# Kernel optimization log

Hardware: AMD Instinct MI355X
Metric: run time of the kernel (lower is better)

The kernel has to match this reference:

```python
import jax, jax.numpy as jnp
import numpy as np

SCALE = 768.0  # scale = output_features


def setup_inputs() -> dict:
    key = jax.random.key(0)
    k1, k2, k3, k4 = jax.random.split(key, 4)
    B, S, D, F = 8, 2048, 768, 768
    x = jax.random.normal(k1, (B, S, D), dtype=jnp.float32)
    # torch nn.Linear weights: shape (out_features, in_features), y = x @ W.T
    Wq = jax.random.normal(k2, (F, D), dtype=jnp.float32) * (1.0 / np.sqrt(D))
    Wk = jax.random.normal(k3, (F, D), dtype=jnp.float32) * (1.0 / np.sqrt(D))
    Wv = jax.random.normal(k4, (F, D), dtype=jnp.float32) * (1.0 / np.sqrt(D))
    return {"x": x, "Wq": Wq, "Wk": Wk, "Wv": Wv}


def _cdist_l2(q, k):
    # pairwise Euclidean distances, [B, S, S]; matches torch.cdist(q, k, p=2)
    q2 = jnp.sum(q * q, axis=-1)  # [B, S]
    k2 = jnp.sum(k * k, axis=-1)  # [B, S]
    qk = jnp.einsum('bid,bjd->bij', q, k)  # [B, S, S]
    d2 = q2[:, :, None] + k2[:, None, :] - 2.0 * qk
    return jnp.sqrt(jnp.maximum(d2, 0.0))


def reference(x, Wq, Wk, Wv):
    q = jnp.einsum('bsd,fd->bsf', x, Wq)
    k = jnp.einsum('bsd,fd->bsf', x, Wk)
    v = jnp.einsum('bsd,fd->bsf', x, Wv)
    scores = _cdist_l2(q, k) / jnp.sqrt(jnp.asarray(SCALE, dtype=x.dtype))
    attn = jax.nn.softmax(scores, axis=-1)  # NOTE: source softmaxes raw distances (no negation)
    return jnp.einsum('bij,bjf->bif', attn, v)
```

## Files before the change

kernel.cpp:

```cpp
#include <hip/hip_runtime.h>
#include <hip/hip_fp8.h>
#include <stdint.h>
#include <math.h>


typedef __attribute__((ext_vector_type(8))) __bf16 bf16x8;
typedef __attribute__((ext_vector_type(4))) float f32x4;
typedef __attribute__((ext_vector_type(4))) unsigned int u32x4;

__device__ __forceinline__ unsigned short f2b(float f) {
    unsigned u = __float_as_uint(f);
    unsigned r = 0x7fffu + ((u >> 16) & 1u);
    return (unsigned short)((u + r) >> 16);
}
__device__ __forceinline__ float b2f(unsigned short h) {
    return __uint_as_float(((unsigned)h) << 16);
}
__device__ __forceinline__ unsigned char f2f8(float f) {
    __hip_fp8_e4m3 t(f);
    return t.__x;
}
__device__ __forceinline__ float f8tof(unsigned char b) {
    int e = (b >> 3) & 15, m = b & 7;
    float v = e ? ldexpf(8.0f + m, e - 10) : ldexpf((float)m, -9);
    return (b & 0x80) ? -v : v;
}

__device__ __forceinline__ void wg_barrier() {
    asm volatile("" ::: "memory");
    __builtin_amdgcn_s_barrier();
    asm volatile("" ::: "memory");
}

__device__ __forceinline__ unsigned lds_off(const void* p) {
    return (unsigned)(uintptr_t)(const __attribute__((address_space(3))) char*)p;
}

__global__ __launch_bounds__(256) void castk(const float* __restrict__ src,
                                             unsigned short* __restrict__ dst, int n4) {
    int i = blockIdx.x * 256 + threadIdx.x;
    if (i >= n4) return;
    float4 v = ((const float4*)src)[i];
    ushort4 o;
    o.x = f2b(v.x); o.y = f2b(v.y); o.z = f2b(v.z); o.w = f2b(v.w);
    ((ushort4*)dst)[i] = o;
}

template <int MODE>
__global__ __launch_bounds__(256) void rowreduce(const unsigned short* __restrict__ X,
                                                 int L, int rows, float* __restrict__ out) {
    int w = threadIdx.x >> 6, lane = threadIdx.x & 63;
    int row = blockIdx.x * 4 + w;
    if (row >= rows) return;
    const unsigned short* xr = X + (size_t)row * L;
    float s = 0.f;
    int passes = L >> 8;
    for (int p = 0; p < passes; ++p) {
        ushort4 u = *(const ushort4*)(xr + (p << 8) + lane * 4);
        float a = b2f(u.x), b = b2f(u.y), c = b2f(u.z), d = b2f(u.w);
        s += MODE ? (a * a + b * b + c * c + d * d) : (a + b + c + d);
    }
#pragma unroll
    for (int o = 32; o > 0; o >>= 1) s += __shfl_down(s, o);
    if (lane == 0) out[row] = s;
}

__global__ __launch_bounds__(256) void rowreduce8(const unsigned char* __restrict__ X,
                                                  int L, int rows, float* __restrict__ out) {
    int w = threadIdx.x >> 6, lane = threadIdx.x & 63;
    int row = blockIdx.x * 4 + w;
    if (row >= rows) return;
    const unsigned char* xr = X + (size_t)row * L;
    float s = 0.f;
    int passes = L >> 8;
    for (int p = 0; p < passes; ++p) {
        uchar4 u = *(const uchar4*)(xr + (p << 8) + lane * 4);
        float a = f8tof(u.x), b = f8tof(u.y), c = f8tof(u.z), d = f8tof(u.w);
        s += a * a + b * b + c * c + d * d;
    }
#pragma unroll
    for (int o = 32; o > 0; o >>= 1) s += __shfl_down(s, o);
    if (lane == 0) out[row] = s;
}

#define MF(A_, B_, C_) (C_) = __builtin_amdgcn_mfma_f32_16x16x32_bf16((A_), (B_), (C_), 0, 0, 0)
#define MF8(A_, B_, C_) (C_) = __builtin_amdgcn_mfma_f32_16x16x32_fp8_fp8((A_), (B_), (C_), 0, 0, 0)
#define DSR(dst_, a_, imm_) \
    asm volatile("ds_read_b128 %0, %1 offset:" #imm_ : "=v"(dst_) : "v"(a_))
#define DSR64(dst_, a_, imm_) \
    asm volatile("ds_read_b64 %0, %1 offset:" #imm_ : "=v"(dst_) : "v"(a_))
#define GL4(d_, p_) asm volatile("global_load_dwordx4 %0, %1, off" : "=v"(d_) : "v"(p_))
#define DSW(a_, imm_, d_) \
    asm volatile("ds_write_b128 %0, %1 offset:" #imm_ :: "v"(a_), "v"(d_) : "memory")
#define LGKM(n_) asm volatile("s_waitcnt lgkmcnt(" #n_ ")" ::: "memory")
#define VMC0 asm volatile("s_waitcnt vmcnt(0)" ::: "memory")
#define SB0 __builtin_amdgcn_sched_barrier(0)

#define LOADT(T_) do {                                                     \
    const size_t ko_ = (size_t)(T_) * 64;                                  \
    GL4(ra0, pa + ko_);             GL4(ra1, pa + lda64 + ko_);            \
    GL4(ra2, pa + 2 * lda64 + ko_); GL4(ra3, pa + 3 * lda64 + ko_);        \
    GL4(rb0, pb + ko_);             GL4(rb1, pb + ldb64 + ko_);            \
    GL4(rb2, pb + 2 * ldb64 + ko_); GL4(rb3, pb + 3 * ldb64 + ko_);        \
} while (0)
#define WRITET(WB_) do {                                                   \
    const unsigned wa_ = wA + (WB_), wb2_ = wB + (WB_);                    \
    DSW(wa_, 0, ra0);     DSW(wa_, 8192, ra1);                             \
    DSW(wa_, 16384, ra2); DSW(wa_, 24576, ra3);                            \
    DSW(wb2_, 0, rb0);     DSW(wb2_, 8192, rb1);                           \
    DSW(wb2_, 16384, rb2); DSW(wb2_, 24576, rb3);                          \
} while (0)

template <int EPI>
__global__ __launch_bounds__(512, 2) void gemm256(
    const unsigned short* __restrict__ A, int lda, long long sA,
    const unsigned short* __restrict__ B, int ldb, long long sB,
    void* __restrict__ Cv, int ldc, long long sC,
    int Kd, int perm,
    const float* __restrict__ aux1, int sAux1) {
    __shared__ __attribute__((aligned(128))) unsigned short As[2 * 256 * 64];
    __shared__ __attribute__((aligned(128))) unsigned short Bs[2 * 256 * 64];

    const int z = perm ? blockIdx.x : blockIdx.z;
    const int jb = perm ? blockIdx.y : blockIdx.x;
    const int ib = perm ? blockIdx.z : blockIdx.y;
    const unsigned short* __restrict__ Ab = A + (size_t)z * sA;
    const unsigned short* __restrict__ Bb = B + (size_t)z * sB;
    const int i0 = ib * 256, j0 = jb * 256;
    const int tid = threadIdx.x;
    const int w = tid >> 6, lane = tid & 63;
    const int wr = w >> 2, wc = w & 3;
    const int c16 = lane & 15, kq = lane >> 4;

    const int lr0 = tid >> 3;
    const int clog0 = (tid & 7) ^ (lr0 & 7);
    const unsigned short* pa = Ab + (size_t)(i0 + lr0) * lda + clog0 * 8;
    const unsigned short* pb = Bb + (size_t)(j0 + lr0) * ldb + clog0 * 8;
    const size_t lda64 = (size_t)64 * lda, ldb64 = (size_t)64 * ldb;

    const unsigned wA = lds_off(As) + (unsigned)tid * 16;
    const unsigned wB = lds_off(Bs) + (unsigned)tid * 16;

    const int swc = (kq ^ (c16 & 7)) << 4;
    const unsigned adrA0 = lds_off(As) + (unsigned)(wr * 128 + c16) * 128 + swc;
    const unsigned adrA0x = adrA0 ^ 64u;
    const unsigned adrB0 = lds_off(Bs) + (unsigned)(wc * 64 + c16) * 128 + swc;
    const unsigned adrB0x = adrB0 ^ 64u;

    f32x4 acc[8][4];
    const f32x4 zero = {0.f, 0.f, 0.f, 0.f};
#pragma unroll
    for (int i = 0; i < 8; ++i)
#pragma unroll
        for (int j = 0; j < 4; ++j) acc[i][j] = zero;

    u32x4 ra0, ra1, ra2, ra3, rb0, rb1, rb2, rb3;
    bf16x8 aL[4][2], aH[4][2], bF[4][2];

    const int nt = Kd >> 6;

    LOADT(0);
    VMC0;
    WRITET(0u);
    LOADT(1);
    LGKM(0);
    wg_barrier();

    for (int t = 0; t < nt; ++t) {
        const unsigned rb_ = (t & 1) ? 32768u : 0u;
        const unsigned wb_ = (t & 1) ? 0u : 32768u;
        const unsigned aA = adrA0 + rb_, aAx = adrA0x + rb_;
        const unsigned aB = adrB0 + rb_, aBx = adrB0x + rb_;
        DSR(aL[0][0], aA, 0);    DSR(aL[0][1], aAx, 0);
        DSR(aL[1][0], aA, 2048); DSR(aL[1][1], aAx, 2048);
        DSR(aL[2][0], aA, 4096); DSR(aL[2][1], aAx, 4096);
        DSR(aL[3][0], aA, 6144); DSR(aL[3][1], aAx, 6144);
        DSR(bF[0][0], aB, 0);    DSR(bF[0][1], aBx, 0);
        DSR(bF[1][0], aB, 2048); DSR(bF[1][1], aBx, 2048);
        DSR(bF[2][0], aB, 4096); DSR(bF[2][1], aBx, 4096);
        DSR(bF[3][0], aB, 6144); DSR(bF[3][1], aBx, 6144);
        if (t + 1 < nt) {
            VMC0;
            WRITET(wb_);
            if (t + 2 < nt) LOADT(t + 2);
            LGKM(8);
        } else {
            LGKM(0);
        }
        SB0;
        __builtin_amdgcn_s_setprio(1);
#pragma unroll
        for (int kk = 0; kk < 2; ++kk)
#pragma unroll
            for (int mi = 0; mi < 4; ++mi)
#pragma unroll
                for (int ni = 0; ni < 4; ++ni)
                    MF(aL[mi][kk], bF[ni][kk], acc[mi][ni]);
        __builtin_amdgcn_s_setprio(0);
        DSR(aH[0][0], aA, 8192);  DSR(aH[0][1], aAx, 8192);
        DSR(aH[1][0], aA, 10240); DSR(aH[1][1], aAx, 10240);
        DSR(aH[2][0], aA, 12288); DSR(aH[2][1], aAx, 12288);
        DSR(aH[3][0], aA, 14336); DSR(aH[3][1], aAx, 14336);
        LGKM(0); SB0;
        __builtin_amdgcn_s_setprio(1);
#pragma unroll
        for (int kk = 0; kk < 2; ++kk)
#pragma unroll
            for (int mi = 0; mi < 4; ++mi)
#pragma unroll
                for (int ni = 0; ni < 4; ++ni)
                    MF(aH[mi][kk], bF[ni][kk], acc[4 + mi][ni]);
        __builtin_amdgcn_s_setprio(0);
        wg_barrier();
    }
    const int prow = kq * 4;
    if constexpr (EPI == 0) {
        unsigned short* C = (unsigned short*)Cv + (size_t)z * sC;
        unsigned short* sc = (unsigned short*)((char*)As + w * 8192);
        const int rr = lane >> 3, ch = lane & 7;
#pragma unroll
        for (int mi = 0; mi < 8; ++mi) {
#pragma unroll
            for (int ni = 0; ni < 4; ++ni)
#pragma unroll
                for (int r = 0; r < 4; ++r)
                    sc[(prow + r) * 72 + ni * 16 + c16] = f2b(acc[mi][ni][r]);
#pragma unroll
            for (int pass = 0; pass < 2; ++pass) {
                const int r2 = rr + 8 * pass;
                bf16x8 v = *(const bf16x8*)&sc[r2 * 72 + ch * 8];
                const int grow = i0 + wr * 128 + mi * 16 + r2;
                *(bf16x8*)&C[(size_t)grow * ldc + j0 + wc * 64 + ch * 8] = v;
            }
        }
    } else if constexpr (EPI == 3) {
        unsigned char* C = (unsigned char*)Cv + (size_t)z * sC;
        unsigned char* sc = (unsigned char*)As + w * 8192;
        const int rr = lane >> 2, ch = lane & 3;
#pragma unroll
        for (int mi = 0; mi < 8; ++mi) {
#pragma unroll
            for (int ni = 0; ni < 4; ++ni)
#pragma unroll
                for (int r = 0; r < 4; ++r)
                    sc[(prow + r) * 80 + ni * 16 + c16] = f2f8(acc[mi][ni][r]);
            u32x4 v = *(const u32x4*)&sc[rr * 80 + ch * 16];
            const int grow = i0 + wr * 128 + mi * 16 + rr;
            *(u32x4*)&C[(size_t)grow * ldc + j0 + wc * 64 + ch * 16] = v;
        }
    } else {
        float* C = (float*)Cv + (size_t)z * sC;
        const float* lb = aux1 + (size_t)z * sAux1;
        float* sc = (float*)((char*)As + w * 8192);
        const int rr = lane >> 4, ch = lane & 15;
#pragma unroll
        for (int mi = 0; mi < 8; ++mi) {
#pragma unroll
            for (int ni = 0; ni < 4; ++ni)
#pragma unroll
                for (int r = 0; r < 4; ++r) {
                    const int grow = i0 + wr * 128 + mi * 16 + prow + r;
                    sc[(prow + r) * 68 + ni * 16 + c16] = acc[mi][ni][r] / lb[grow];
                }
#pragma unroll
            for (int pass = 0; pass < 4; ++pass) {
                const int r2 = rr + 4 * pass;
                f32x4 v = *(const f32x4*)&sc[r2 * 68 + ch * 4];
                const int grow = i0 + wr * 128 + mi * 16 + r2;
                *(f32x4*)&C[(size_t)grow * ldc + j0 + wc * 64 + ch * 4] = v;
            }
        }
    }
}

#define LOADT8(T_) do {                                                    \
    const size_t ko_ = (size_t)(T_) * 64;                                  \
    GL4(fa0, pa8 + ko_);                                                   \
    GL4(fb0, pb8 + ko_); GL4(fb1, pb8 + ldb128 + ko_);                     \
} while (0)
#define WRITET8(WB_) do {                                                  \
    DSW(wA8 + ((WB_) >> 1), 0, fa0);                                       \
    DSW(wB8 + (WB_), 0, fb0); DSW(wB8 + (WB_), 8192, fb1);                 \
} while (0)

__global__ __launch_bounds__(512, 4) void gemm256f8(
    const unsigned char* __restrict__ A, int lda, long long sA,
    const unsigned char* __restrict__ B, int ldb, long long sB,
    unsigned short* __restrict__ Cq, int ldc, long long sC,
    int Kd,
    const float* __restrict__ q2a, int sQ2,
    const float* __restrict__ k2a, int sK2,
    float invs) {
    __shared__ __attribute__((aligned(128))) unsigned char As8[2 * 128 * 64];
    __shared__ __attribute__((aligned(128))) unsigned char Bs8[2 * 256 * 64];

    const int z = blockIdx.x;
    const int jb = blockIdx.y, ib = blockIdx.z;
    const unsigned char* __restrict__ Ab = A + (size_t)z * sA;
    const unsigned char* __restrict__ Bb = B + (size_t)z * sB;
    const int i0 = ib * 128, j0 = jb * 256;
    const int tid = threadIdx.x;
    const int w = tid >> 6, lane = tid & 63;
    const int wr = w >> 2, wc = w & 3;
    const int c16 = lane & 15, kq = lane >> 4;

    const int srow = tid >> 2;
    const int p8 = (tid & 3) ^ (srow & 3) ^ ((srow >> 2) & 1);
    const unsigned char* pa8 = Ab + (size_t)(i0 + srow) * lda + p8 * 16;
    const unsigned char* pb8 = Bb + (size_t)(j0 + srow) * ldb + p8 * 16;
    const size_t ldb128 = (size_t)128 * ldb;

    const unsigned wA8 = lds_off(As8) + (unsigned)tid * 16;
    const unsigned wB8 = lds_off(Bs8) + (unsigned)tid * 16;

    const int gl = (c16 & 3) ^ ((c16 >> 2) & 1);
    const int soff = ((((kq >> 1) ^ gl) << 4) | ((kq & 1) << 3));
    const unsigned adrA80 = lds_off(As8) + (unsigned)(wr * 64 + c16) * 64 + soff;
    const unsigned adrB80 = lds_off(Bs8) + (unsigned)(wc * 64 + c16) * 64 + soff;

    f32x4 acc[4][4];
    const f32x4 zero = {0.f, 0.f, 0.f, 0.f};
#pragma unroll
    for (int i = 0; i < 4; ++i)
#pragma unroll
        for (int j = 0; j < 4; ++j) acc[i][j] = zero;

    u32x4 fa0, fb0, fb1;
    long aF[4][2], bF[4][2];

    const int nt = Kd >> 6;

    LOADT8(0);
    VMC0;
    WRITET8(0u);
    LOADT8(1);
    LGKM(0);
    wg_barrier();

    for (int t = 0; t < nt; ++t) {
        const unsigned rb_ = (t & 1) ? 16384u : 0u;
        const unsigned wb_ = (t & 1) ? 0u : 16384u;
        const unsigned aA = adrA80 + (rb_ >> 1), aAx = aA ^ 32u;
        const unsigned aB = adrB80 + rb_, aBx = aB ^ 32u;
        DSR64(aF[0][0], aA, 0);    DSR64(aF[0][1], aAx, 0);
        DSR64(aF[1][0], aA, 1024); DSR64(aF[1][1], aAx, 1024);
        DSR64(aF[2][0], aA, 2048); DSR64(aF[2][1], aAx, 2048);
        DSR64(aF[3][0], aA, 3072); DSR64(aF[3][1], aAx, 3072);
        DSR64(bF[0][0], aB, 0);    DSR64(bF[0][1], aBx, 0);
        DSR64(bF[1][0], aB, 1024); DSR64(bF[1][1], aBx, 1024);
        DSR64(bF[2][0], aB, 2048); DSR64(bF[2][1], aBx, 2048);
        DSR64(bF[3][0], aB, 3072); DSR64(bF[3][1], aBx, 3072);
        if (t + 1 < nt) {
            VMC0;
            WRITET8(wb_);
            if (t + 2 < nt) LOADT8(t + 2);
            LGKM(3);
        } else {
            LGKM(0);
        }
        SB0;
        __builtin_amdgcn_s_setprio(1);
#pragma unroll
        for (int kk = 0; kk < 2; ++kk)
#pragma unroll
            for (int mi = 0; mi < 4; ++mi)
#pragma unroll
                for (int ni = 0; ni < 4; ++ni)
                    MF8(aF[mi][kk], bF[ni][kk], acc[mi][ni]);
        __builtin_amdgcn_s_setprio(0);
        LGKM(0);
        wg_barrier();
    }

    unsigned short* C = Cq + (size_t)z * sC;
    const float* q2b = q2a + (size_t)z * sQ2;
    const float* k2b = k2a + (size_t)z * sK2;
    unsigned short* sc = (unsigned short*)(Bs8 + w * 4096);
    const int prow = kq * 4;
    const int rr = lane >> 3, ch = lane & 7;
#pragma unroll
    for (int mi = 0; mi < 4; ++mi) {
#pragma unroll
        for (int ni = 0; ni < 4; ++ni) {
            const int col = j0 + wc * 64 + ni * 16 + c16;
            const float k2v = k2b[col];
#pragma unroll
            for (int r = 0; r < 4; ++r) {
                const int grow = i0 + wr * 64 + mi * 16 + prow + r;
                float d2 = q2b[grow] + k2v - 2.0f * acc[mi][ni][r];
                float e = __expf(sqrtf(fmaxf(d2, 0.f)) * invs);
                sc[(prow + r) * 72 + ni * 16 + c16] = f2b(e);
            }
        }
#pragma unroll
        for (int pass = 0; pass < 2; ++pass) {
            const int r2 = rr + 8 * pass;
            bf16x8 v = *(const bf16x8*)&sc[r2 * 72 + ch * 8];
            const int grow = i0 + wr * 64 + mi * 16 + r2;
            *(bf16x8*)&C[(size_t)grow * ldc + j0 + wc * 64 + ch * 8] = v;
        }
    }
}

extern "C" void kernel_launch(void* const* d_in, const int* in_sizes, int n_in,
                              void* d_out, int out_size, void* d_ws, size_t ws_size,
                              hipStream_t stream) {
    const float* x = (const float*)d_in[0];
    const float* Wq = (const float*)d_in[1];
    const float* Wk = (const float*)d_in[2];
    const float* Wv = (const float*)d_in[3];
    const int Bz = 8, S = 2048, D = 768, F = 768;
    const int BS = Bz * S;

    const size_t szX = (size_t)BS * D * 2;
    const size_t szW = (size_t)F * D * 2;
    const size_t szQ8 = (size_t)BS * F;
    const size_t szE = (size_t)Bz * S * S * 2;

    char* p = (char*)d_ws;
    unsigned short* xb = (unsigned short*)p;  p += szX;
    unsigned short* Wqb = (unsigned short*)p; p += szW;
    unsigned short* Wkb = (unsigned short*)p; p += szW;
    unsigned short* Wvb = (unsigned short*)p; p += szW;
    unsigned char* Q8 = (unsigned char*)p;    p += szQ8;
    unsigned char* K8 = (unsigned char*)p;    p += szQ8;
    unsigned short* VT = (unsigned short*)p;  p += szX;
    unsigned short* E = (unsigned short*)p;   p += szE;
    float* q2 = (float*)p;    p += (size_t)BS * 4;
    float* k2 = (float*)p;    p += (size_t)BS * 4;
    float* lsum = (float*)p;  p += (size_t)BS * 4;
    if ((size_t)(p - (char*)d_ws) > ws_size) return;

    const float invs = 1.0f / sqrtf(768.0f);

    castk<<<(BS * D / 4 + 255) / 256, 256, 0, stream>>>(x, xb, BS * D / 4);
    castk<<<(F * D / 4 + 255) / 256, 256, 0, stream>>>(Wq, Wqb, F * D / 4);
    castk<<<(F * D / 4 + 255) / 256, 256, 0, stream>>>(Wk, Wkb, F * D / 4);
    castk<<<(F * D / 4 + 255) / 256, 256, 0, stream>>>(Wv, Wvb, F * D / 4);

    gemm256<3><<<dim3(F / 256, BS / 256, 2), 512, 0, stream>>>(
        xb, D, 0,
        Wqb, D, (long long)F * D,
        Q8, F, (long long)BS * F,
        D, 0, nullptr, 0);

    gemm256<0><<<dim3(BS / 256, F / 256, 1), 512, 0, stream>>>(
        Wvb, D, 0,
        xb, D, 0,
        VT, BS, 0,
        D, 0, nullptr, 0);

    rowreduce8<<<BS / 4, 256, 0, stream>>>(Q8, F, BS, q2);
    rowreduce8<<<BS / 4, 256, 0, stream>>>(K8, F, BS, k2);

    gemm256f8<<<dim3(Bz, S / 256, S / 128), 512, 0, stream>>>(
        Q8, F, (long long)S * F,
        K8, F, (long long)S * F,
        E, S, (long long)S * S,
        F, q2, S, k2, S, invs);

    rowreduce<0><<<BS / 4, 256, 0, stream>>>(E, S, BS, lsum);

    gemm256<2><<<dim3(Bz, F / 256, S / 256), 512, 0, stream>>>(
        E, S, (long long)S * S,
        VT, BS, (long long)S,
        d_out, F, (long long)S * F,
        S, 1, lsum, S);
}
```

Before: 233.1 us.

## Replace 256x256 bf16 GEMM with 128x256 tile, K=32 steps, higher occupancy

Rewrites the bf16 GEMM kernel to use 128x256 output tiles with 32-wide K steps and a smaller LDS footprint, raising launch bounds to 4 blocks per CU. The epilogues drop the LDS staging and write accumulators straight to global memory. The final GEMM multiplies by a precomputed reciprocal instead of dividing. This aims to raise occupancy and the number of blocks for the smaller grids, but it costs less register reuse per block, twice as many barriers per K, and uncoalesced scattered scalar stores in the epilogue.

```diff
diff --git a/kernel.cpp b/kernel.cpp
--- a/kernel.cpp
+++ b/kernel.cpp
@@ -96,178 +96,138 @@
 #define VMC0 asm volatile("s_waitcnt vmcnt(0)" ::: "memory")
 #define SB0 __builtin_amdgcn_sched_barrier(0)
 
-#define LOADT(T_) do {                                                     \
-    const size_t ko_ = (size_t)(T_) * 64;                                  \
-    GL4(ra0, pa + ko_);             GL4(ra1, pa + lda64 + ko_);            \
-    GL4(ra2, pa + 2 * lda64 + ko_); GL4(ra3, pa + 3 * lda64 + ko_);        \
-    GL4(rb0, pb + ko_);             GL4(rb1, pb + ldb64 + ko_);            \
-    GL4(rb2, pb + 2 * ldb64 + ko_); GL4(rb3, pb + 3 * ldb64 + ko_);        \
+#define LOADTB(T_) do {                                                    \
+    const size_t ko_ = (size_t)(T_) * 32;                                  \
+    GL4(ra0, pa + ko_);                                                    \
+    GL4(rb0, pb + ko_); GL4(rb1, pb + ldb128 + ko_);                       \
 } while (0)
-#define WRITET(WB_) do {                                                   \
-    const unsigned wa_ = wA + (WB_), wb2_ = wB + (WB_);                    \
-    DSW(wa_, 0, ra0);     DSW(wa_, 8192, ra1);                             \
-    DSW(wa_, 16384, ra2); DSW(wa_, 24576, ra3);                            \
-    DSW(wb2_, 0, rb0);     DSW(wb2_, 8192, rb1);                           \
-    DSW(wb2_, 16384, rb2); DSW(wb2_, 24576, rb3);                          \
+#define WRITETB(WB_) do {                                                  \
+    DSW(wAa + ((WB_) >> 1), 0, ra0);                                       \
+    DSW(wBb + (WB_), 0, rb0); DSW(wBb + (WB_), 8192, rb1);                 \
 } while (0)
 
 template <int EPI>
-__global__ __launch_bounds__(512, 2) void gemm256(
+__global__ __launch_bounds__(512, 4) void gemm128b(
     const unsigned short* __restrict__ A, int lda, long long sA,
     const unsigned short* __restrict__ B, int ldb, long long sB,
     void* __restrict__ Cv, int ldc, long long sC,
     int Kd, int perm,
     const float* __restrict__ aux1, int sAux1) {
-    __shared__ __attribute__((aligned(128))) unsigned short As[2 * 256 * 64];
-    __shared__ __attribute__((aligned(128))) unsigned short Bs[2 * 256 * 64];
+    __shared__ __attribute__((aligned(128))) unsigned short As[2 * 128 * 32];
+    __shared__ __attribute__((aligned(128))) unsigned short Bs[2 * 256 * 32];
 
     const int z = perm ? blockIdx.x : blockIdx.z;
     const int jb = perm ? blockIdx.y : blockIdx.x;
     const int ib = perm ? blockIdx.z : blockIdx.y;
     const unsigned short* __restrict__ Ab = A + (size_t)z * sA;
     const unsigned short* __restrict__ Bb = B + (size_t)z * sB;
-    const int i0 = ib * 256, j0 = jb * 256;
+    const int i0 = ib * 128, j0 = jb * 256;
     const int tid = threadIdx.x;
     const int w = tid >> 6, lane = tid & 63;
     const int wr = w >> 2, wc = w & 3;
     const int c16 = lane & 15, kq = lane >> 4;
 
-    const int lr0 = tid >> 3;
-    const int clog0 = (tid & 7) ^ (lr0 & 7);
-    const unsigned short* pa = Ab + (size_t)(i0 + lr0) * lda + clog0 * 8;
-    const unsigned short* pb = Bb + (size_t)(j0 + lr0) * ldb + clog0 * 8;
-    const size_t lda64 = (size_t)64 * lda, ldb64 = (size_t)64 * ldb;
-
-    const unsigned wA = lds_off(As) + (unsigned)tid * 16;
-    const unsigned wB = lds_off(Bs) + (unsigned)tid * 16;
-
-    const int swc = (kq ^ (c16 & 7)) << 4;
-    const unsigned adrA0 = lds_off(As) + (unsigned)(wr * 128 + c16) * 128 + swc;
-    const unsigned adrA0x = adrA0 ^ 64u;
-    const unsigned adrB0 = lds_off(Bs) + (unsigned)(wc * 64 + c16) * 128 + swc;
-    const unsigned adrB0x = adrB0 ^ 64u;
-
-    f32x4 acc[8][4];
+    const int srow = tid >> 2;
+    const int clog = (tid & 3) ^ ((srow >> 1) & 3);
+    const unsigned short* pa = Ab + (size_t)(i0 + srow) * lda + clog * 8;
+    const unsigned short* pb = Bb + (size_t)(j0 + srow) * ldb + clog * 8;
+    const size_t ldb128 = (size_t)128 * ldb;
+
+    const unsigned wAa = lds_off(As) + (unsigned)tid * 16;
+    const unsigned wBb = lds_off(Bs) + (unsigned)tid * 16;
+
+    const int sw = (kq ^ ((c16 >> 1) & 3)) << 4;
+    const unsigned adrA0 = lds_off(As) + (unsigned)(wr * 64 + c16) * 64 + sw;
+    const unsigned adrB0 = lds_off(Bs) + (unsigned)(wc * 64 + c16) * 64 + sw;
+
+    f32x4 acc[4][4];
     const f32x4 zero = {0.f, 0.f, 0.f, 0.f};
 #pragma unroll
-    for (int i = 0; i < 8; ++i)
+    for (int i = 0; i < 4; ++i)
 #pragma unroll
         for (int j = 0; j < 4; ++j) acc[i][j] = zero;
 
-    u32x4 ra0, ra1, ra2, ra3, rb0, rb1, rb2, rb3;
-    bf16x8 aL[4][2], aH[4][2], bF[4][2];
-
-    const int nt = Kd >> 6;
-
-    LOADT(0);
+    u32x4 ra0, rb0, rb1;
+    bf16x8 aF[4], bF[4];
+
+    const int nt = Kd >> 5;
+
+    LOADTB(0);
     VMC0;
-    WRITET(0u);
-    LOADT(1);
+    WRITETB(0u);
+    LOADTB(1);
     LGKM(0);
     wg_barrier();
 
     for (int t = 0; t < nt; ++t) {
-        const unsigned rb_ = (t & 1) ? 32768u : 0u;
-        const unsigned wb_ = (t & 1) ? 0u : 32768u;
-        const unsigned aA = adrA0 + rb_, aAx = adrA0x + rb_;
-        const unsigned aB = adrB0 + rb_, aBx = adrB0x + rb_;
-        DSR(aL[0][0], aA, 0);    DSR(aL[0][1], aAx, 0);
-        DSR(aL[1][0], aA, 2048); DSR(aL[1][1], aAx, 2048);
-        DSR(aL[2][0], aA, 4096); DSR(aL[2][1], aAx, 4096);
-        DSR(aL[3][0], aA, 6144); DSR(aL[3][1], aAx, 6144);
-        DSR(bF[0][0], aB, 0);    DSR(bF[0][1], aBx, 0);
-        DSR(bF[1][0], aB, 2048); DSR(bF[1][1], aBx, 2048);
-        DSR(bF[2][0], aB, 4096); DSR(bF[2][1], aBx, 4096);
-        DSR(bF[3][0], aB, 6144); DSR(bF[3][1], aBx, 6144);
+        const unsigned rb_ = (t & 1) ? 16384u : 0u;
+        const unsigned wb_ = (t & 1) ? 0u : 16384u;
+        const unsigned aA = adrA0 + (rb_ >> 1);
+        const unsigned aB = adrB0 + rb_;
+        DSR(aF[0], aA, 0);    DSR(aF[1], aA, 1024);
+        DSR(aF[2], aA, 2048); DSR(aF[3], aA, 3072);
+        DSR(bF[0], aB, 0);    DSR(bF[1], aB, 1024);
+        DSR(bF[2], aB, 2048); DSR(bF[3], aB, 3072);
         if (t + 1 < nt) {
             VMC0;
-            WRITET(wb_);
-            if (t + 2 < nt) LOADT(t + 2);
-            LGKM(8);
+            WRITETB(wb_);
+            if (t + 2 < nt) LOADTB(t + 2);
+            LGKM(3);
         } else {
             LGKM(0);
         }
         SB0;
         __builtin_amdgcn_s_setprio(1);
 #pragma unroll
-        for (int kk = 0; kk < 2; ++kk)
-#pragma unroll
-            for (int mi = 0; mi < 4; ++mi)
-#pragma unroll
-                for (int ni = 0; ni < 4; ++ni)
-                    MF(aL[mi][kk], bF[ni][kk], acc[mi][ni]);
+        for (int mi = 0; mi < 4; ++mi)
+#pragma unroll
+            for (int ni = 0; ni < 4; ++ni)
+                MF(aF[mi], bF[ni], acc[mi][ni]);
         __builtin_amdgcn_s_setprio(0);
-        DSR(aH[0][0], aA, 8192);  DSR(aH[0][1], aAx, 8192);
-        DSR(aH[1][0], aA, 10240); DSR(aH[1][1], aAx, 10240);
-        DSR(aH[2][0], aA, 12288); DSR(aH[2][1], aAx, 12288);
-        DSR(aH[3][0], aA, 14336); DSR(aH[3][1], aAx, 14336);
-        LGKM(0); SB0;
-        __builtin_amdgcn_s_setprio(1);
-#pragma unroll
-        for (int kk = 0; kk < 2; ++kk)
-#pragma unroll
-            for (int mi = 0; mi < 4; ++mi)
-#pragma unroll
-                for (int ni = 0; ni < 4; ++ni)
-                    MF(aH[mi][kk], bF[ni][kk], acc[4 + mi][ni]);
-        __builtin_amdgcn_s_setprio(0);
+        LGKM(0);
         wg_barrier();
     }
+
     const int prow = kq * 4;
     if constexpr (EPI == 0) {
         unsigned short* C = (unsigned short*)Cv + (size_t)z * sC;
-        unsigned short* sc = (unsigned short*)((char*)As + w * 8192);
-        const int rr = lane >> 3, ch = lane & 7;
-#pragma unroll
-        for (int mi = 0; mi < 8; ++mi) {
-#pragma unroll
-            for (int ni = 0; ni < 4; ++ni)
+#pragma unroll
+        for (int mi = 0; mi < 4; ++mi)
+#pragma unroll
+            for (int ni = 0; ni < 4; ++ni) {
+                const int row = i0 + wr * 64 + mi * 16 + prow;
+                const int col = j0 + wc * 64 + ni * 16 + c16;
 #pragma unroll
                 for (int r = 0; r < 4; ++r)
-                    sc[(prow + r) * 72 + ni * 16 + c16] = f2b(acc[mi][ni][r]);
-#pragma unroll
-            for (int pass = 0; pass < 2; ++pass) {
-                const int r2 = rr + 8 * pass;
-                bf16x8 v = *(const bf16x8*)&sc[r2 * 72 + ch * 8];
-                const int grow = i0 + wr * 128 + mi * 16 + r2;
-                *(bf16x8*)&C[(size_t)grow * ldc + j0 + wc * 64 + ch * 8] = v;
+                    C[(size_t)(row + r) * ldc + col] = f2b(acc[mi][ni][r]);
             }
-        }
     } else if constexpr (EPI == 3) {
         unsigned char* C = (unsigned char*)Cv + (size_t)z * sC;
-        unsigned char* sc = (unsigned char*)As + w * 8192;
-        const int rr = lane >> 2, ch = lane & 3;
-#pragma unroll
-        for (int mi = 0; mi < 8; ++mi) {
-#pragma unroll
-            for (int ni = 0; ni < 4; ++ni)
+#pragma unroll
+        for (int mi = 0; mi < 4; ++mi)
+#pragma unroll
+            for (int ni = 0; ni < 4; ++ni) {
+                const int row = i0 + wr * 64 + mi * 16 + prow;
+                const int col = j0 + wc * 64 + ni * 16 + c16;
 #pragma unroll
                 for (int r = 0; r < 4; ++r)
-                    sc[(prow + r) * 80 + ni * 16 + c16] = f2f8(acc[mi][ni][r]);
-            u32x4 v = *(const u32x4*)&sc[rr * 80 + ch * 16];
-            const int grow = i0 + wr * 128 + mi * 16 + rr;
-            *(u32x4*)&C[(size_t)grow * ldc + j0 + wc * 64 + ch * 16] = v;
-        }
+                    C[(size_t)(row + r) * ldc + col] = f2f8(acc[mi][ni][r]);
+            }
     } else {
         float* C = (float*)Cv + (size_t)z * sC;
         const float* lb = aux1 + (size_t)z * sAux1;
-        float* sc = (float*)((char*)As + w * 8192);
-        const int rr = lane >> 4, ch = lane & 15;
-#pragma unroll
-        for (int mi = 0; mi < 8; ++mi) {
-#pragma unroll
-            for (int ni = 0; ni < 4; ++ni)
-#pragma unroll
-                for (int r = 0; r < 4; ++r) {
-                    const int grow = i0 + wr * 128 + mi * 16 + prow + r;
-                    sc[(prow + r) * 68 + ni * 16 + c16] = acc[mi][ni][r] / lb[grow];
-                }
-#pragma unroll
-            for (int pass = 0; pass < 4; ++pass) {
-                const int r2 = rr + 4 * pass;
-                f32x4 v = *(const f32x4*)&sc[r2 * 68 + ch * 4];
-                const int grow = i0 + wr * 128 + mi * 16 + r2;
-                *(f32x4*)&C[(size_t)grow * ldc + j0 + wc * 64 + ch * 4] = v;
+#pragma unroll
+        for (int mi = 0; mi < 4; ++mi) {
+            const int row = i0 + wr * 64 + mi * 16 + prow;
+            float linv[4];
+#pragma unroll
+            for (int r = 0; r < 4; ++r) linv[r] = 1.0f / lb[row + r];
+#pragma unroll
+            for (int ni = 0; ni < 4; ++ni) {
+                const int col = j0 + wc * 64 + ni * 16 + c16;
+#pragma unroll
+                for (int r = 0; r < 4; ++r)
+                    C[(size_t)(row + r) * ldc + col] = acc[mi][ni][r] * linv[r];
             }
         }
     }
@@ -438,13 +398,13 @@
     castk<<<(F * D / 4 + 255) / 256, 256, 0, stream>>>(Wk, Wkb, F * D / 4);
     castk<<<(F * D / 4 + 255) / 256, 256, 0, stream>>>(Wv, Wvb, F * D / 4);
 
-    gemm256<3><<<dim3(F / 256, BS / 256, 2), 512, 0, stream>>>(
+    gemm128b<3><<<dim3(F / 256, BS / 128, 2), 512, 0, stream>>>(
         xb, D, 0,
         Wqb, D, (long long)F * D,
         Q8, F, (long long)BS * F,
         D, 0, nullptr, 0);
 
-    gemm256<0><<<dim3(BS / 256, F / 256, 1), 512, 0, stream>>>(
+    gemm128b<0><<<dim3(BS / 256, F / 128, 1), 512, 0, stream>>>(
         Wvb, D, 0,
         xb, D, 0,
         VT, BS, 0,
@@ -461,7 +421,7 @@
 
     rowreduce<0><<<BS / 4, 256, 0, stream>>>(E, S, BS, lsum);
 
-    gemm256<2><<<dim3(Bz, F / 256, S / 256), 512, 0, stream>>>(
+    gemm128b<2><<<dim3(Bz, F / 256, S / 128), 512, 0, stream>>>(
         E, S, (long long)S * S,
         VT, BS, (long long)S,
         d_out, F, (long long)S * F,
```

Result: no change. 234.9 us (+0.8%).
